# Optimization experiments

Measured on AMD Instinct MI355X. Metric: run time of the kernel, lower is better.

## Reference

```python
import jax, jax.numpy as jnp
import numpy as np

B, T, D, F_FF, E, K = 8, 2048, 1024, 4096, 8, 2


def setup_inputs() -> dict:
    key = jax.random.key(0)
    ks = jax.random.split(key, 6)
    s = 1.0 / np.sqrt(D)
    return {
        "x": jax.random.normal(ks[0], (B, T, D), jnp.float32),
        "Wr": jax.random.normal(ks[1], (D, E), jnp.float32) * s,
        "W1": jax.random.normal(ks[2], (E, D, F_FF), jnp.float32) * s,
        "b1": jax.random.normal(ks[3], (E, F_FF), jnp.float32) * 0.01,
        "W2": jax.random.normal(ks[4], (E, F_FF, D), jnp.float32) * (1.0 / np.sqrt(F_FF)),
        "b2": jax.random.normal(ks[5], (E, D), jnp.float32) * 0.01,
    }


def reference(x, Wr, W1, b1, W2, b2):
    # Per-SAMPLE routing (matches original: top_idx is (B, K), whole sequence
    # x[b] is processed by the selected expert, scaled by scalar weights[b,k]).
    pooled = x.mean(axis=1)                       # (B, D)
    logits = pooled @ Wr                          # (B, E)
    top_scores, top_idx = jax.lax.top_k(logits, K)  # (B, K)
    weights = jax.nn.softmax(top_scores, axis=-1)   # (B, K)

    # Gather each selected expert's FFN params: (B, K, ...)
    W1s, b1s = W1[top_idx], b1[top_idx]
    W2s, b2s = W2[top_idx], b2[top_idx]

    h = jnp.einsum('btd,bkdf->bktf', x, W1s) + b1s[:, :, None, :]
    h = jax.nn.gelu(h, approximate=False)         # torch F.gelu default = erf
    y = jnp.einsum('bktf,bkfd->bktd', h, W2s) + b2s[:, :, None, :]
    out = jnp.einsum('bk,bktd->btd', weights, y)  # weighted combine
    return out
```

## Files before the change

### kernel.cpp

```cpp
#include <hip/hip_runtime.h>

#define T_SEQ 2048
#define DDIM  1024
#define FDIM  4096
#define NE    8

typedef __attribute__((ext_vector_type(8))) __bf16 bf16x8;
typedef __attribute__((ext_vector_type(4))) float  f32x4;

__device__ __forceinline__ void gld16(const void* g, void* l) {
    __builtin_amdgcn_global_load_lds(
        (__attribute__((address_space(1))) void*)g,
        (__attribute__((address_space(3))) void*)l,
        16, 0, 0);
}

__global__ void kpool(const float* __restrict__ x, float* __restrict__ part) {
    int bd = blockIdx.x * 256 + threadIdx.x;
    int tc = blockIdx.y;
    int b = bd >> 10;
    int d = bd & 1023;
    const float* p = x + ((size_t)b * T_SEQ + (size_t)tc * 256) * DDIM + d;
    float s = 0.f;
    #pragma unroll 8
    for (int t = 0; t < 256; ++t) s += p[(size_t)t * DDIM];
    part[tc * 8192 + bd] = s;
}

__global__ void kroute(const float* __restrict__ part, const float* __restrict__ Wr,
                       int* __restrict__ ridx, float* __restrict__ rw) {
    __shared__ float pooled[8192];
    __shared__ float plg[256];
    __shared__ float lg[64];
    int tid = threadIdx.x;
    for (int i = tid; i < 8192; i += 256) {
        float s = 0.f;
        #pragma unroll
        for (int tc = 0; tc < 8; ++tc) s += part[tc * 8192 + i];
        pooled[i] = s * (1.0f / (float)T_SEQ);
    }
    __syncthreads();
    {
        int b = tid >> 5, e = (tid >> 2) & 7, q = tid & 3;
        float s = 0.f;
        const float* pb = pooled + b * 1024 + q * 256;
        for (int d = 0; d < 256; ++d) s += pb[d] * Wr[(q * 256 + d) * NE + e];
        plg[tid] = s;
    }
    __syncthreads();
    if (tid < 64) {
        int b = tid >> 3, e = tid & 7;
        int base = b * 32 + e * 4;
        lg[tid] = plg[base] + plg[base + 1] + plg[base + 2] + plg[base + 3];
    }
    __syncthreads();
    if (tid < 8) {
        int b = tid;
        float best = -1e30f; int bi = 0;
        #pragma unroll
        for (int e = 0; e < 8; ++e) { float v = lg[b * 8 + e]; if (v > best) { best = v; bi = e; } }
        float best2 = -1e30f; int bi2 = 0;
        #pragma unroll
        for (int e = 0; e < 8; ++e) {
            if (e == bi) continue;
            float v = lg[b * 8 + e];
            if (v > best2) { best2 = v; bi2 = e; }
        }
        float e1 = __expf(best2 - best);
        float inv = 1.0f / (1.0f + e1);
        ridx[b * 2]     = bi;
        ridx[b * 2 + 1] = bi2;
        rw[b * 2]     = inv;
        rw[b * 2 + 1] = e1 * inv;
    }
}

__global__ void kconvX(const float* __restrict__ in, __bf16* __restrict__ out) {
    size_t i = ((size_t)blockIdx.x * 256 + threadIdx.x) * 4;
    float4 v = *(const float4*)(in + i);
    union { __bf16 h[4]; uint2 u; } pk;
    pk.h[0] = (__bf16)v.x; pk.h[1] = (__bf16)v.y;
    pk.h[2] = (__bf16)v.z; pk.h[3] = (__bf16)v.w;
    *(uint2*)(out + i) = pk.u;
}

__global__ void kconvT(const float* __restrict__ in, __bf16* __restrict__ out,
                       int R, int C) {
    __shared__ float t[64][65];
    int e  = blockIdx.z;
    int r0 = blockIdx.y * 64;
    int c0 = blockIdx.x * 64;
    int tid = threadIdx.x;
    const float* ip = in + ((size_t)e * R + r0) * C + c0;
    int tr  = tid >> 4;
    int tc4 = (tid & 15) * 4;
    #pragma unroll
    for (int j = 0; j < 4; ++j) {
        float4 v = *(const float4*)(ip + (size_t)(tr + j * 16) * C + tc4);
        t[tr + j * 16][tc4 + 0] = v.x;
        t[tr + j * 16][tc4 + 1] = v.y;
        t[tr + j * 16][tc4 + 2] = v.z;
        t[tr + j * 16][tc4 + 3] = v.w;
    }
    __syncthreads();
    __bf16* op = out + ((size_t)e * C + c0) * R + r0;
    int oc  = tid >> 2;
    int orb = (tid & 3) * 16;
    #pragma unroll
    for (int s = 0; s < 4; ++s) {
        int orr = orb + s * 4;
        union { __bf16 h[4]; uint2 u; } pk;
        pk.h[0] = (__bf16)t[orr + 0][oc];
        pk.h[1] = (__bf16)t[orr + 1][oc];
        pk.h[2] = (__bf16)t[orr + 2][oc];
        pk.h[3] = (__bf16)t[orr + 3][oc];
        *(uint2*)(op + (size_t)oc * R + orr) = pk.u;
    }
}

__device__ __forceinline__ void mma256(
    const __bf16* __restrict__ A, const __bf16* __restrict__ B, int K,
    __bf16* __restrict__ lds,
    f32x4 (&acc)[8][4], int m0, int n0)
{
    const int tid = threadIdx.x;
    const int l  = tid & 63;
    const int w  = tid >> 6;
    const int lr = l & 15;
    const int lq = l >> 4;
    const int wm = w >> 2;
    const int wn = w & 3;

    const __bf16* gA[4]; const __bf16* gB[4];
    int lo[4];
    #pragma unroll
    for (int i = 0; i < 4; ++i) {
        int s   = w * 4 + i;
        int row = ((s >> 1) << 4) + lr;
        int k   = ((s & 1) << 5) + (lq << 3);
        gA[i] = A + (size_t)(m0 + row) * K + k;
        gB[i] = B + (size_t)(n0 + row) * K + k;
        lo[i] = s * 512 + l * 8;
    }

    const int nt = K >> 6;

    #pragma unroll
    for (int i = 0; i < 4; ++i) {
        gld16(gA[i], lds + lo[i]);
        gld16(gB[i], lds + 16384 + lo[i]);
    }

    for (int t = 0; t < nt; ++t) {
        __bf16* cur = lds + (t & 1) * 32768;
        if (t + 1 < nt) {
            __bf16* nxt = lds + ((t + 1) & 1) * 32768;
            const int koff = (t + 1) << 6;
            #pragma unroll
            for (int i = 0; i < 4; ++i) {
                gld16(gA[i] + koff, nxt + lo[i]);
                gld16(gB[i] + koff, nxt + 16384 + lo[i]);
            }
            asm volatile("s_waitcnt vmcnt(8)" ::: "memory");
        } else {
            asm volatile("s_waitcnt vmcnt(0)" ::: "memory");
        }
        asm volatile("s_barrier" ::: "memory");
        #pragma unroll
        for (int kk = 0; kk < 2; ++kk) {
            bf16x8 af[8], bfr[4];
            #pragma unroll
            for (int im = 0; im < 8; ++im) {
                int s = ((wm * 8 + im) << 1) + kk;
                af[im] = *(const bf16x8*)(cur + s * 512 + l * 8);
            }
            #pragma unroll
            for (int jn = 0; jn < 4; ++jn) {
                int s = ((wn * 4 + jn) << 1) + kk;
                bfr[jn] = *(const bf16x8*)(cur + 16384 + s * 512 + l * 8);
            }
            #pragma unroll
            for (int im = 0; im < 8; ++im)
                #pragma unroll
                for (int jn = 0; jn < 4; ++jn)
                    acc[im][jn] = __builtin_amdgcn_mfma_f32_16x16x32_bf16(
                        af[im], bfr[jn], acc[im][jn], 0, 0, 0);
        }
        asm volatile("s_barrier" ::: "memory");
    }
}

__global__ __launch_bounds__(512, 2) void gemm1_kernel(
    const __bf16* __restrict__ xbf, const __bf16* __restrict__ W1t,
    const float* __restrict__ b1, const int* __restrict__ ridx,
    const float* __restrict__ rw, __bf16* __restrict__ h, int p0)
{
    __shared__ __attribute__((aligned(16))) __bf16 lds[65536];
    const int lp = blockIdx.z;
    const int p  = p0 + lp;
    const int b  = p >> 1;
    const int e  = ridx[p];
    const float wgt = rw[p];
    const int m0 = blockIdx.y * 256;
    const int n0 = blockIdx.x * 256;

    f32x4 acc[8][4];
    #pragma unroll
    for (int i = 0; i < 8; ++i)
        #pragma unroll
        for (int j = 0; j < 4; ++j)
            acc[i][j] = (f32x4){0.f, 0.f, 0.f, 0.f};

    mma256(xbf + (size_t)b * T_SEQ * DDIM, W1t + (size_t)e * FDIM * DDIM,
           DDIM, lds, acc, m0, n0);

    const int l  = threadIdx.x & 63;
    const int w  = threadIdx.x >> 6;
    const int wmo = (w >> 2) << 7, wno = (w & 3) << 6;
    const int lr = l & 15, lq = l >> 4;
    __bf16* hd = h + (size_t)lp * T_SEQ * FDIM;
    const float* bias = b1 + e * FDIM;
    #pragma unroll
    for (int im = 0; im < 8; ++im) {
        int row = m0 + wmo + im * 16 + lq * 4;
        #pragma unroll
        for (int jn = 0; jn < 4; ++jn) {
            int col = n0 + wno + jn * 16 + lr;
            float bv = bias[col];
            #pragma unroll
            for (int r = 0; r < 4; ++r) {
                float v = acc[im][jn][r] + bv;
                v = 0.5f * v * (1.0f + erff(v * 0.70710678118654752f));
                hd[(size_t)(row + r) * FDIM + col] = (__bf16)(wgt * v);
            }
        }
    }
}

__global__ __launch_bounds__(512, 2) void gemm2_kernel(
    const __bf16* __restrict__ h, const __bf16* __restrict__ W2t,
    const float* __restrict__ b2, const int* __restrict__ ridx,
    const float* __restrict__ rw, float* __restrict__ out, int s0)
{
    __shared__ __attribute__((aligned(16))) __bf16 lds[65536];
    const int ls = blockIdx.z;
    const int s  = s0 + ls;
    const int e0 = ridx[s * 2], e1 = ridx[s * 2 + 1];
    const float w0 = rw[s * 2], w1 = rw[s * 2 + 1];
    const int m0 = blockIdx.y * 256;
    const int n0 = blockIdx.x * 256;

    f32x4 acc[8][4];
    #pragma unroll
    for (int i = 0; i < 8; ++i)
        #pragma unroll
        for (int j = 0; j < 4; ++j)
            acc[i][j] = (f32x4){0.f, 0.f, 0.f, 0.f};

    mma256(h + (size_t)(2 * ls) * T_SEQ * FDIM, W2t + (size_t)e0 * DDIM * FDIM,
           FDIM, lds, acc, m0, n0);
    mma256(h + (size_t)(2 * ls + 1) * T_SEQ * FDIM, W2t + (size_t)e1 * DDIM * FDIM,
           FDIM, lds, acc, m0, n0);

    const int l  = threadIdx.x & 63;
    const int w  = threadIdx.x >> 6;
    const int wmo = (w >> 2) << 7, wno = (w & 3) << 6;
    const int lr = l & 15, lq = l >> 4;
    float* od = out + (size_t)s * T_SEQ * DDIM;
    const float* bb0 = b2 + e0 * DDIM;
    const float* bb1 = b2 + e1 * DDIM;
    #pragma unroll
    for (int im = 0; im < 8; ++im) {
        int row = m0 + wmo + im * 16 + lq * 4;
        #pragma unroll
        for (int jn = 0; jn < 4; ++jn) {
            int col = n0 + wno + jn * 16 + lr;
            float bv = w0 * bb0[col] + w1 * bb1[col];
            #pragma unroll
            for (int r = 0; r < 4; ++r)
                od[(size_t)(row + r) * DDIM + col] = acc[im][jn][r] + bv;
        }
    }
}

extern "C" void kernel_launch(void* const* d_in, const int* in_sizes, int n_in,
                              void* d_out, int out_size, void* d_ws, size_t ws_size,
                              hipStream_t stream) {
    const float* x  = (const float*)d_in[0];
    const float* Wr = (const float*)d_in[1];
    const float* W1 = (const float*)d_in[2];
    const float* b1 = (const float*)d_in[3];
    const float* W2 = (const float*)d_in[4];
    const float* b2 = (const float*)d_in[5];
    float* out = (float*)d_out;
    char*  ws  = (char*)d_ws;

    int*    ridx = (int*)(ws + 0);
    float*  rw   = (float*)(ws + 64);
    float*  part = (float*)(ws + 1024);
    __bf16* xbf  = (__bf16*)(ws + ((size_t)1  << 20));
    __bf16* W1t  = (__bf16*)(ws + ((size_t)33 << 20));
    __bf16* W2t  = (__bf16*)(ws + ((size_t)97 << 20));
    __bf16* hbuf = (__bf16*)(ws + ((size_t)161 << 20));

    kpool <<<dim3(32, 8), 256, 0, stream>>>(x, part);
    kroute<<<1, 256, 0, stream>>>(part, Wr, ridx, rw);
    kconvX<<<16384, 256, 0, stream>>>(x, xbf);
    kconvT<<<dim3(FDIM / 64, DDIM / 64, NE), 256, 0, stream>>>(W1, W1t, DDIM, FDIM);
    kconvT<<<dim3(DDIM / 64, FDIM / 64, NE), 256, 0, stream>>>(W2, W2t, FDIM, DDIM);

    const size_t h_per_sample = (size_t)2 * T_SEQ * FDIM * sizeof(__bf16);
    size_t hcap = (ws_size > ((size_t)161 << 20)) ? ws_size - ((size_t)161 << 20) : 0;
    int csmax = (int)(hcap / h_per_sample);
    if (csmax < 1) csmax = 1;
    if (csmax > 8) csmax = 8;

    for (int smp0 = 0; smp0 < 8; smp0 += csmax) {
        int cs = (8 - smp0 < csmax) ? (8 - smp0) : csmax;
        gemm1_kernel<<<dim3(FDIM / 256, T_SEQ / 256, 2 * cs), 512, 0, stream>>>(
            xbf, W1t, b1, ridx, rw, hbuf, smp0 * 2);
        gemm2_kernel<<<dim3(DDIM / 256, T_SEQ / 256, cs), 512, 0, stream>>>(
            hbuf, W2t, b2, ridx, rw, out, smp0);
    }
}
```

Measured before the change: 1.181 ms.

## Split GEMM main loop into four phases interleaving LDS reads, global prefetch, MFMA

Restructures the shared 256x256 MFMA mainloop into four sub-phases per K-tile. Each phase loads a slice of A fragments from LDS, issues part of the next tile's global-to-LDS prefetch, and runs a block of MFMAs raised to high priority with s_setprio. B fragments are held in registers across the whole tile, and the B prefetch runs two tiles ahead into the buffer that frees up. K becomes a template parameter so the loop count is constant. The aim is to spread memory traffic across the compute and cut register pressure from holding all 8 A fragments at once, at the cost of more barriers per iteration and tricky buffer-reuse timing.

```diff
diff --git a/kernel.cpp b/kernel.cpp
--- a/kernel.cpp
+++ b/kernel.cpp
@@ -118,11 +118,13 @@
     }
 }
 
+template<int K>
 __device__ __forceinline__ void mma256(
-    const __bf16* __restrict__ A, const __bf16* __restrict__ B, int K,
+    const __bf16* __restrict__ A, const __bf16* __restrict__ B,
     __bf16* __restrict__ lds,
     f32x4 (&acc)[8][4], int m0, int n0)
 {
+    constexpr int nt = K >> 6;
     const int tid = threadIdx.x;
     const int l  = tid & 63;
     const int w  = tid >> 6;
@@ -131,62 +133,152 @@
     const int wm = w >> 2;
     const int wn = w & 3;
 
-    const __bf16* gA[4]; const __bf16* gB[4];
-    int lo[4];
-    #pragma unroll
-    for (int i = 0; i < 4; ++i) {
-        int s   = w * 4 + i;
-        int row = ((s >> 1) << 4) + lr;
-        int k   = ((s & 1) << 5) + (lq << 3);
-        gA[i] = A + (size_t)(m0 + row) * K + k;
-        gB[i] = B + (size_t)(n0 + row) * K + k;
-        lo[i] = s * 512 + l * 8;
-    }
-
-    const int nt = K >> 6;
-
-    #pragma unroll
-    for (int i = 0; i < 4; ++i) {
-        gld16(gA[i], lds + lo[i]);
-        gld16(gB[i], lds + 16384 + lo[i]);
-    }
-
+    long aoff[2], boff[2];
+    int  lA[2],  lB[2];
+    #pragma unroll
+    for (int j = 0; j < 2; ++j) {
+        aoff[j] = (long)(m0 + (w << 4) + lr) * K + (j << 5) + (lq << 3);
+        boff[j] = (long)(n0 + (w << 4) + lr) * K + (j << 5) + (lq << 3);
+        lA[j] = (2 * w + j) * 512 + l * 8;
+        lB[j] = 16384 + (2 * w + j) * 512 + l * 8;
+    }
+    const long rhalf = (long)128 * K;
+
+    const int afo = wm * 8 * 1024 + l * 8;
+    const int bfo = 16384 + wn * 4 * 1024 + l * 8;
+
+    #pragma unroll
+    for (int j = 0; j < 2; ++j) {
+        gld16(A + aoff[j],         lds + lA[j]);
+        gld16(A + aoff[j] + rhalf, lds + lA[j] + 8192);
+        gld16(B + boff[j],         lds + lB[j]);
+        gld16(B + boff[j] + rhalf, lds + lB[j] + 8192);
+    }
+    if (nt > 1) {
+        __bf16* d1 = lds + 32768;
+        #pragma unroll
+        for (int j = 0; j < 2; ++j) {
+            gld16(B + boff[j] + 64,         d1 + lB[j]);
+            gld16(B + boff[j] + rhalf + 64, d1 + lB[j] + 8192);
+        }
+        asm volatile("s_waitcnt vmcnt(4)" ::: "memory");
+    } else {
+        asm volatile("s_waitcnt vmcnt(0)" ::: "memory");
+    }
+    __builtin_amdgcn_s_barrier();
+
+    bf16x8 bfr[4][2];
     for (int t = 0; t < nt; ++t) {
-        __bf16* cur = lds + (t & 1) * 32768;
+        const __bf16* cur = lds + (t & 1) * 32768;
+        __bf16* nx1 = lds + ((t + 1) & 1) * 32768;
+        __bf16* nx2 = lds + (t & 1) * 32768;
+        const long ko1 = (long)(t + 1) << 6;
+        const long ko2 = (long)(t + 2) << 6;
+
+        bf16x8 af[2][2];
+
+        #pragma unroll
+        for (int kk = 0; kk < 2; ++kk) {
+            af[0][kk] = *(const bf16x8*)(cur + afo + 0 * 1024 + kk * 512);
+            af[1][kk] = *(const bf16x8*)(cur + afo + 1 * 1024 + kk * 512);
+            #pragma unroll
+            for (int jn = 0; jn < 4; ++jn)
+                bfr[jn][kk] = *(const bf16x8*)(cur + bfo + jn * 1024 + kk * 512);
+        }
         if (t + 1 < nt) {
-            __bf16* nxt = lds + ((t + 1) & 1) * 32768;
-            const int koff = (t + 1) << 6;
-            #pragma unroll
-            for (int i = 0; i < 4; ++i) {
-                gld16(gA[i] + koff, nxt + lo[i]);
-                gld16(gB[i] + koff, nxt + 16384 + lo[i]);
+            #pragma unroll
+            for (int j = 0; j < 2; ++j)
+                gld16(A + aoff[j] + ko1, nx1 + lA[j]);
+        }
+        __builtin_amdgcn_s_barrier();
+        asm volatile("s_waitcnt lgkmcnt(0)" ::: "memory");
+        __builtin_amdgcn_sched_barrier(0);
+        __builtin_amdgcn_s_setprio(1);
+        #pragma unroll
+        for (int kk = 0; kk < 2; ++kk)
+            #pragma unroll
+            for (int jn = 0; jn < 4; ++jn) {
+                acc[0][jn] = __builtin_amdgcn_mfma_f32_16x16x32_bf16(af[0][kk], bfr[jn][kk], acc[0][jn], 0, 0, 0);
+                acc[1][jn] = __builtin_amdgcn_mfma_f32_16x16x32_bf16(af[1][kk], bfr[jn][kk], acc[1][jn], 0, 0, 0);
             }
-            asm volatile("s_waitcnt vmcnt(8)" ::: "memory");
-        } else {
-            asm volatile("s_waitcnt vmcnt(0)" ::: "memory");
-        }
-        asm volatile("s_barrier" ::: "memory");
+        __builtin_amdgcn_s_setprio(0);
+        __builtin_amdgcn_s_barrier();
+
         #pragma unroll
         for (int kk = 0; kk < 2; ++kk) {
-            bf16x8 af[8], bfr[4];
-            #pragma unroll
-            for (int im = 0; im < 8; ++im) {
-                int s = ((wm * 8 + im) << 1) + kk;
-                af[im] = *(const bf16x8*)(cur + s * 512 + l * 8);
+            af[0][kk] = *(const bf16x8*)(cur + afo + 2 * 1024 + kk * 512);
+            af[1][kk] = *(const bf16x8*)(cur + afo + 3 * 1024 + kk * 512);
+        }
+        if (t + 1 < nt) {
+            #pragma unroll
+            for (int j = 0; j < 2; ++j)
+                gld16(A + aoff[j] + rhalf + ko1, nx1 + lA[j] + 8192);
+        }
+        __builtin_amdgcn_s_barrier();
+        asm volatile("s_waitcnt lgkmcnt(0)" ::: "memory");
+        __builtin_amdgcn_sched_barrier(0);
+        __builtin_amdgcn_s_setprio(1);
+        #pragma unroll
+        for (int kk = 0; kk < 2; ++kk)
+            #pragma unroll
+            for (int jn = 0; jn < 4; ++jn) {
+                acc[2][jn] = __builtin_amdgcn_mfma_f32_16x16x32_bf16(af[0][kk], bfr[jn][kk], acc[2][jn], 0, 0, 0);
+                acc[3][jn] = __builtin_amdgcn_mfma_f32_16x16x32_bf16(af[1][kk], bfr[jn][kk], acc[3][jn], 0, 0, 0);
             }
+        __builtin_amdgcn_s_setprio(0);
+        __builtin_amdgcn_s_barrier();
+
+        #pragma unroll
+        for (int kk = 0; kk < 2; ++kk) {
+            af[0][kk] = *(const bf16x8*)(cur + afo + 4 * 1024 + kk * 512);
+            af[1][kk] = *(const bf16x8*)(cur + afo + 5 * 1024 + kk * 512);
+        }
+        if (t + 2 < nt) {
+            #pragma unroll
+            for (int j = 0; j < 2; ++j)
+                gld16(B + boff[j] + ko2, nx2 + lB[j]);
+        }
+        __builtin_amdgcn_s_barrier();
+        asm volatile("s_waitcnt lgkmcnt(0)" ::: "memory");
+        __builtin_amdgcn_sched_barrier(0);
+        __builtin_amdgcn_s_setprio(1);
+        #pragma unroll
+        for (int kk = 0; kk < 2; ++kk)
             #pragma unroll
             for (int jn = 0; jn < 4; ++jn) {
-                int s = ((wn * 4 + jn) << 1) + kk;
-                bfr[jn] = *(const bf16x8*)(cur + 16384 + s * 512 + l * 8);
+                acc[4][jn] = __builtin_amdgcn_mfma_f32_16x16x32_bf16(af[0][kk], bfr[jn][kk], acc[4][jn], 0, 0, 0);
+                acc[5][jn] = __builtin_amdgcn_mfma_f32_16x16x32_bf16(af[1][kk], bfr[jn][kk], acc[5][jn], 0, 0, 0);
             }
-            #pragma unroll
-            for (int im = 0; im < 8; ++im)
-                #pragma unroll
-                for (int jn = 0; jn < 4; ++jn)
-                    acc[im][jn] = __builtin_amdgcn_mfma_f32_16x16x32_bf16(
-                        af[im], bfr[jn], acc[im][jn], 0, 0, 0);
-        }
-        asm volatile("s_barrier" ::: "memory");
+        __builtin_amdgcn_s_setprio(0);
+        __builtin_amdgcn_s_barrier();
+
+        #pragma unroll
+        for (int kk = 0; kk < 2; ++kk) {
+            af[0][kk] = *(const bf16x8*)(cur + afo + 6 * 1024 + kk * 512);
+            af[1][kk] = *(const bf16x8*)(cur + afo + 7 * 1024 + kk * 512);
+        }
+        if (t + 2 < nt) {
+            #pragma unroll
+            for (int j = 0; j < 2; ++j)
+                gld16(B + boff[j] + rhalf + ko2, nx2 + lB[j] + 8192);
+        }
+        __builtin_amdgcn_s_barrier();
+        asm volatile("s_waitcnt lgkmcnt(0)" ::: "memory");
+        __builtin_amdgcn_sched_barrier(0);
+        __builtin_amdgcn_s_setprio(1);
+        #pragma unroll
+        for (int kk = 0; kk < 2; ++kk)
+            #pragma unroll
+            for (int jn = 0; jn < 4; ++jn) {
+                acc[6][jn] = __builtin_amdgcn_mfma_f32_16x16x32_bf16(af[0][kk], bfr[jn][kk], acc[6][jn], 0, 0, 0);
+                acc[7][jn] = __builtin_amdgcn_mfma_f32_16x16x32_bf16(af[1][kk], bfr[jn][kk], acc[7][jn], 0, 0, 0);
+            }
+        __builtin_amdgcn_s_setprio(0);
+        if (t + 1 < nt) {
+            if (t + 2 < nt) asm volatile("s_waitcnt vmcnt(4)" ::: "memory");
+            else            asm volatile("s_waitcnt vmcnt(0)" ::: "memory");
+        }
+        __builtin_amdgcn_s_barrier();
     }
 }
 
@@ -211,8 +303,8 @@
         for (int j = 0; j < 4; ++j)
             acc[i][j] = (f32x4){0.f, 0.f, 0.f, 0.f};
 
-    mma256(xbf + (size_t)b * T_SEQ * DDIM, W1t + (size_t)e * FDIM * DDIM,
-           DDIM, lds, acc, m0, n0);
+    mma256<DDIM>(xbf + (size_t)b * T_SEQ * DDIM, W1t + (size_t)e * FDIM * DDIM,
+                 lds, acc, m0, n0);
 
     const int l  = threadIdx.x & 63;
     const int w  = threadIdx.x >> 6;
@@ -257,10 +349,10 @@
         for (int j = 0; j < 4; ++j)
             acc[i][j] = (f32x4){0.f, 0.f, 0.f, 0.f};
 
-    mma256(h + (size_t)(2 * ls) * T_SEQ * FDIM, W2t + (size_t)e0 * DDIM * FDIM,
-           FDIM, lds, acc, m0, n0);
-    mma256(h + (size_t)(2 * ls + 1) * T_SEQ * FDIM, W2t + (size_t)e1 * DDIM * FDIM,
-           FDIM, lds, acc, m0, n0);
+    mma256<FDIM>(h + (size_t)(2 * ls) * T_SEQ * FDIM, W2t + (size_t)e0 * DDIM * FDIM,
+                 lds, acc, m0, n0);
+    mma256<FDIM>(h + (size_t)(2 * ls + 1) * T_SEQ * FDIM, W2t + (size_t)e1 * DDIM * FDIM,
+                 lds, acc, m0, n0);
 
     const int l  = threadIdx.x & 63;
     const int w  = threadIdx.x >> 6;
```

Measured after the change: 1.072 ms. 1.1x faster.
